# Kernel optimization log

Measured on AMD Instinct MI355X. Metric: run time of the kernel, lower is better.

## Reference

```python
import jax, jax.numpy as jnp
import numpy as np

N = 100000      # n_nodes
E = 1600000     # n_edges (avg degree 16)
F_IN = 128      # nfeat
H = 128         # nhid
C = 64          # nclass


def setup_inputs() -> dict:
    key = jax.random.key(0)
    ks = jax.random.split(key, 6)
    x = jax.random.normal(ks[0], (N, F_IN), dtype=jnp.float32)
    edge_index = jax.random.randint(ks[1], (2, E), 0, N, dtype=jnp.int32)
    # Glorot-ish init for GCNConv weights, zeros for bias (PyG default)
    W1 = jax.random.normal(ks[2], (F_IN, H), dtype=jnp.float32) * (1.0 / np.sqrt(F_IN))
    b1 = jnp.zeros((H,), dtype=jnp.float32)
    W2 = jax.random.normal(ks[3], (H, C), dtype=jnp.float32) * (1.0 / np.sqrt(H))
    b2 = jnp.zeros((C,), dtype=jnp.float32)
    return {"x": x, "edge_index": edge_index, "W1": W1, "b1": b1, "W2": W2, "b2": b2}


def _gcn_conv(x, W, b, src, dst, n):
    """PyG GCNConv: h = W^T x, out_i = sum_j norm_ij * h_j + b, with
    symmetric normalization over the self-loop-augmented graph."""
    h = x @ W                                                   # [n, out]
    deg = jax.ops.segment_sum(jnp.ones(src.shape[0], h.dtype), dst, num_segments=n)
    dinv = jnp.where(deg > 0, jax.lax.rsqrt(deg), 0.0)          # D^-1/2
    norm = dinv[src] * dinv[dst]                                # [E+n]
    msg = h[src] * norm[:, None]                                # gather + scale
    out = jax.ops.segment_sum(msg, dst, num_segments=n)         # scatter-add
    return out + b


def reference(x, edge_index, W1, b1, W2, b2):
    loop = jnp.arange(N, dtype=edge_index.dtype)
    src = jnp.concatenate([edge_index[0], loop])  # sources j (with self loops)
    dst = jnp.concatenate([edge_index[1], loop])  # targets i
    h = jax.nn.relu(_gcn_conv(x, W1, b1, src, dst, N))  # dropout = identity (eval)
    out = _gcn_conv(h, W2, b2, src, dst, N)
    return jax.nn.log_softmax(out, axis=1)
```

## Files before the change

kernel.cpp:

```cpp
#include <hip/hip_runtime.h>
#include <hip/hip_fp16.h>
#include <cstdint>
#include <cstddef>
#include <cstring>


__device__ inline unsigned pack_bf16x2(float a, float b) {
    unsigned ua = __float_as_uint(a);
    unsigned ub = __float_as_uint(b);
    ua += 0x7fffu + ((ua >> 16) & 1u);
    ub += 0x7fffu + ((ub >> 16) & 1u);
    return (ua >> 16) | (ub & 0xffff0000u);
}
__device__ inline unsigned short bf16_rne(float v) {
    unsigned u = __float_as_uint(v);
    u += 0x7fffu + ((u >> 16) & 1u);
    return (unsigned short)(u >> 16);
}
__device__ inline float bf16lo(unsigned u) { return __uint_as_float(u << 16); }
__device__ inline float bf16hi(unsigned u) { return __uint_as_float(u & 0xffff0000u); }


typedef float fv2 __attribute__((ext_vector_type(2)));

template <bool HI>
__device__ inline fv2 fp8_fv2(unsigned u) {
#if __has_builtin(__builtin_amdgcn_cvt_pk_f32_fp8)
    return __builtin_amdgcn_cvt_pk_f32_fp8((int)u, HI);
#else
    unsigned u2 = HI ? (u >> 16) : (u & 0xffffu);
    unsigned w = (u2 & 0xFFu) | ((u2 & 0xFF00u) << 8);
    unsigned hb = ((w & 0x00800080u) << 8) | ((w & 0x007f007fu) << 7);
    __half2 h2;
    memcpy(&h2, &hb, 4);
    float2 f = __half22float2(h2);
    fv2 r;
    r.x = f.x * 256.0f;
    r.y = f.y * 256.0f;
    return r;
#endif
}

__device__ inline fv2 bfpair(unsigned u) {
    union { unsigned q[2]; fv2 f; } t;
    t.q[0] = u << 16;
    t.q[1] = u & 0xffff0000u;
    return t.f;
}

__device__ inline unsigned f32_to_fp8_byte(float v) {
    unsigned short hb = __half_as_ushort(__float2half(v * 0.00390625f));
    unsigned t = hb & 0x7fffu;
    t += 0x3fu + ((t >> 7) & 1u);
    return ((hb >> 8) & 0x80u) | (t >> 7);
}

__device__ inline unsigned char f32_to_fp8_b(float v) {
#if __has_builtin(__builtin_amdgcn_cvt_pk_fp8_f32)
    return (unsigned char)(__builtin_amdgcn_cvt_pk_fp8_f32(v, v, 0, false) & 0xff);
#else
    return (unsigned char)f32_to_fp8_byte(v);
#endif
}

__device__ inline fv2 red2(fv2 v) {
    v.x += __shfl_xor(v.x, 16);
    v.y += __shfl_xor(v.y, 16);
    v.x += __shfl_xor(v.x, 32);
    v.y += __shfl_xor(v.y, 32);
    return v;
}

typedef int iv4 __attribute__((ext_vector_type(4)));

#define NPART 8
#define KB    32
#define NPP_MAX 12500


__global__ void k_zero16(int* __restrict__ p) {
    if (threadIdx.x < 16) p[threadIdx.x] = 0;
}

__global__ __launch_bounds__(256) void k_bcount(const int* __restrict__ dst,
                                                int* __restrict__ bucketCount,
                                                int E, int npp) {
    __shared__ int c8[NPART];
    if (threadIdx.x < NPART) c8[threadIdx.x] = 0;
    __syncthreads();
    int t = blockIdx.x * blockDim.x + threadIdx.x;
    int stride = gridDim.x * blockDim.x;
    int E4 = E >> 2;
    const iv4* d4 = (const iv4*)dst;
    for (int i = t; i < E4; i += stride) {
        iv4 d = d4[i];
        atomicAdd(&c8[(unsigned)d.x / (unsigned)npp], 1);
        atomicAdd(&c8[(unsigned)d.y / (unsigned)npp], 1);
        atomicAdd(&c8[(unsigned)d.z / (unsigned)npp], 1);
        atomicAdd(&c8[(unsigned)d.w / (unsigned)npp], 1);
    }
    for (int e = E4 * 4 + t; e < E; e += stride)
        atomicAdd(&c8[(unsigned)dst[e] / (unsigned)npp], 1);
    __syncthreads();
    if (threadIdx.x < NPART) atomicAdd(&bucketCount[threadIdx.x], c8[threadIdx.x]);
}

__global__ void k_bscan(const int* __restrict__ bucketCount,
                        int* __restrict__ bucketBase,
                        int* __restrict__ bucketCursor) {
    if (threadIdx.x == 0) {
        int run = 0;
        for (int p = 0; p < NPART; ++p) {
            bucketBase[p] = run;
            bucketCursor[p] = run;
            run += bucketCount[p];
        }
    }
}

__global__ __launch_bounds__(256) void k_bucket(const int* __restrict__ src,
                                                const int* __restrict__ dst,
                                                int* __restrict__ bucketCursor,
                                                int2* __restrict__ pairs,
                                                int E, int npp) {
    __shared__ int cnt8[NPART], run8[NPART], gbase8[NPART];
    int tid = threadIdx.x;
    int base_e = blockIdx.x * 4096 + tid * 16;
    int nv = min(16, E - base_e);
    if (nv < 0) nv = 0;
    int dv[16], sv[16];
    if (nv == 16) {
        for (int q = 0; q < 4; ++q) {
            iv4 d = *(const iv4*)(dst + base_e + q * 4);
            iv4 s = *(const iv4*)(src + base_e + q * 4);
            dv[q * 4 + 0] = d.x; dv[q * 4 + 1] = d.y; dv[q * 4 + 2] = d.z; dv[q * 4 + 3] = d.w;
            sv[q * 4 + 0] = s.x; sv[q * 4 + 1] = s.y; sv[q * 4 + 2] = s.z; sv[q * 4 + 3] = s.w;
        }
    } else {
        for (int k = 0; k < nv; ++k) { dv[k] = dst[base_e + k]; sv[k] = src[base_e + k]; }
    }
    if (tid < NPART) { cnt8[tid] = 0; run8[tid] = 0; }
    __syncthreads();
    for (int k = 0; k < nv; ++k)
        atomicAdd(&cnt8[(unsigned)dv[k] / (unsigned)npp], 1);
    __syncthreads();
    if (tid < NPART) gbase8[tid] = atomicAdd(&bucketCursor[tid], cnt8[tid]);
    __syncthreads();
    for (int k = 0; k < nv; ++k) {
        int p = (unsigned)dv[k] / (unsigned)npp;
        int r = atomicAdd(&run8[p], 1);
        int2 pr; pr.x = dv[k]; pr.y = sv[k];
        pairs[gbase8[p] + r] = pr;
    }
}

__global__ __launch_bounds__(256) void k_count_part(const int2* __restrict__ pairs,
                                                    const int* __restrict__ bucketBase,
                                                    const int* __restrict__ bucketCount,
                                                    int* __restrict__ cntarr, int npp) {
    __shared__ int h[NPP_MAX];
    int p = blockIdx.x & (NPART - 1);
    int b = blockIdx.x >> 3;
    int lo = p * npp;
    for (int i = threadIdx.x; i < npp; i += 256) h[i] = 0;
    __syncthreads();
    int segBase = bucketBase[p], sz = bucketCount[p];
    int chunk = (sz + KB - 1) / KB;
    int s0 = segBase + b * chunk;
    int s1 = min(segBase + sz, s0 + chunk);
    for (int i = s0 + threadIdx.x; i < s1; i += 256)
        atomicAdd(&h[pairs[i].x - lo], 1);
    __syncthreads();
    size_t out = (size_t)(p * KB + b) * npp;
    for (int i = threadIdx.x; i < npp; i += 256) cntarr[out + i] = h[i];
}

__global__ void k_indeg(const int* __restrict__ cntarr, int* __restrict__ indeg,
                        int n, int npp) {
    int d = blockIdx.x * blockDim.x + threadIdx.x;
    if (d >= n) return;
    int p = (unsigned)d / (unsigned)npp;
    int dl = d - p * npp;
    size_t base = (size_t)p * KB * npp + dl;
    int s = 0;
    for (int b = 0; b < KB; ++b) s += cntarr[base + (size_t)b * npp];
    indeg[d] = s;
}

__global__ void k_scan_local(const int* __restrict__ in, int* __restrict__ out,
                             int* __restrict__ partials, int n) {
    __shared__ int s[256];
    int t = threadIdx.x;
    int base = blockIdx.x * 1024 + t * 4;
    int v0 = (base + 0) < n ? in[base + 0] : 0;
    int v1 = (base + 1) < n ? in[base + 1] : 0;
    int v2 = (base + 2) < n ? in[base + 2] : 0;
    int v3 = (base + 3) < n ? in[base + 3] : 0;
    int sum = v0 + v1 + v2 + v3;
    s[t] = sum;
    __syncthreads();
    for (int off = 1; off < 256; off <<= 1) {
        int x = (t >= off) ? s[t - off] : 0;
        __syncthreads();
        s[t] += x;
        __syncthreads();
    }
    int excl = s[t] - sum;
    if ((base + 0) < n) out[base + 0] = excl;
    if ((base + 1) < n) out[base + 1] = excl + v0;
    if ((base + 2) < n) out[base + 2] = excl + v0 + v1;
    if ((base + 3) < n) out[base + 3] = excl + v0 + v1 + v2;
    if (t == 255) partials[blockIdx.x] = s[255];
}

__global__ void k_scan_partials(int* __restrict__ partials, int np) {
    __shared__ int s[256];
    int t = threadIdx.x;
    int v = (t < np) ? partials[t] : 0;
    s[t] = v;
    __syncthreads();
    for (int off = 1; off < 256; off <<= 1) {
        int x = (t >= off) ? s[t - off] : 0;
        __syncthreads();
        s[t] += x;
        __syncthreads();
    }
    if (t < np) partials[t] = s[t] - v;
}

__global__ void k_finalize(int* __restrict__ row_ptr, const int* __restrict__ partials,
                           const int* __restrict__ indeg, float* __restrict__ dinv,
                           int n, int E) {
    int i = blockIdx.x * blockDim.x + threadIdx.x;
    if (i < n) {
        int rp = row_ptr[i] + partials[i >> 10];
        row_ptr[i] = rp;
        dinv[i] = rsqrtf((float)indeg[i] + 1.0f);
        if (i == 0) row_ptr[n] = E;
    }
}

__global__ void k_bases(int* __restrict__ cntarr, const int* __restrict__ row_ptr,
                        int n, int npp) {
    int d = blockIdx.x * blockDim.x + threadIdx.x;
    if (d >= n) return;
    int p = (unsigned)d / (unsigned)npp;
    int dl = d - p * npp;
    size_t base = (size_t)p * KB * npp + dl;
    int run = row_ptr[d];
    for (int b = 0; b < KB; ++b) {
        size_t idx = base + (size_t)b * npp;
        int c = cntarr[idx];
        cntarr[idx] = run;
        run += c;
    }
}

__global__ __launch_bounds__(256) void k_fill2(const int2* __restrict__ pairs,
                                               const int* __restrict__ bucketBase,
                                               const int* __restrict__ bucketCount,
                                               const int* __restrict__ cntarr,
                                               int* __restrict__ col, int npp) {
    __shared__ int cur[NPP_MAX];
    int p = blockIdx.x & (NPART - 1);
    int b = blockIdx.x >> 3;
    int lo = p * npp;
    size_t slice = (size_t)(p * KB + b) * npp;
    for (int i = threadIdx.x; i < npp; i += 256) cur[i] = cntarr[slice + i];
    __syncthreads();
    int segBase = bucketBase[p], sz = bucketCount[p];
    int chunk = (sz + KB - 1) / KB;
    int s0 = segBase + b * chunk;
    int s1 = min(segBase + sz, s0 + chunk);
    for (int i = s0 + threadIdx.x; i < s1; i += 256) {
        int2 e = pairs[i];
        int pos = atomicAdd(&cur[e.x - lo], 1);
        col[pos] = e.y;
    }
}

typedef __attribute__((ext_vector_type(8))) short short8;
typedef __attribute__((ext_vector_type(4))) float f32x4;

union FragU {
    short8 s;
    uint4 u4;
    unsigned u[4];
};

template <int NOUT>
__global__ void k_packW(const float* __restrict__ W, unsigned* __restrict__ Bp) {
    const int NT = NOUT / 16;
    int nf = 4 * NT * 64;
    for (int fid = threadIdx.x; fid < nf; fid += 256) {
        int q = fid / (NT * 64);
        int rem = fid - q * NT * 64;
        int nt = rem >> 6;
        int lane = rem & 63;
        int k0 = q * 32 + (lane >> 4) * 8;
        int ncol = nt * 16 + (lane & 15);
        unsigned u[4];
        for (int h = 0; h < 4; ++h) {
            float a = W[(k0 + 2 * h) * NOUT + ncol];
            float b = W[(k0 + 2 * h + 1) * NOUT + ncol];
            u[h] = pack_bf16x2(a, b);
        }
        uint4 o = {u[0], u[1], u[2], u[3]};
        *(uint4*)(Bp + (size_t)fid * 4) = o;
    }
}

__global__ __launch_bounds__(256) void k_gemm128_mfma(const float* __restrict__ X,
                                                      const unsigned* __restrict__ Bp,
                                                      const float* __restrict__ dinv,
                                                      unsigned char* __restrict__ H8,
                                                      int n) {
    int w = threadIdx.x >> 6;
    int lane = threadIdx.x & 63;
    int quad = lane >> 4;
    int lrow = lane & 15;
    int row0 = blockIdx.x * 64 + w * 16;
    int rowA = min(row0 + lrow, n - 1);

    f32x4 acc[8];
    for (int nt = 0; nt < 8; ++nt) acc[nt] = (f32x4){0.f, 0.f, 0.f, 0.f};

    for (int q = 0; q < 4; ++q) {
        const float* xp = X + (size_t)rowA * 128 + q * 32 + quad * 8;
        float4 x0 = *(const float4*)xp;
        float4 x1 = *(const float4*)(xp + 4);
        FragU a;
        a.u[0] = pack_bf16x2(x0.x, x0.y);
        a.u[1] = pack_bf16x2(x0.z, x0.w);
        a.u[2] = pack_bf16x2(x1.x, x1.y);
        a.u[3] = pack_bf16x2(x1.z, x1.w);
        for (int nt = 0; nt < 8; ++nt) {
            FragU b;
            b.u4 = *(const uint4*)(Bp + ((size_t)(q * 8 + nt) * 64 + lane) * 4);
            acc[nt] = __builtin_amdgcn_mfma_f32_16x16x32_bf16(a.s, b.s, acc[nt], 0, 0, 0);
        }
    }

    int rbase = row0 + quad * 4;
    float dv[4];
    if (rbase + 3 < n) {
        float4 d4 = *(const float4*)(dinv + rbase);
        dv[0] = d4.x; dv[1] = d4.y; dv[2] = d4.z; dv[3] = d4.w;
    } else {
        for (int r = 0; r < 4; ++r) dv[r] = dinv[min(rbase + r, n - 1)];
    }
    for (int nt = 0; nt < 8; ++nt) {
        for (int r = 0; r < 4; ++r) {
            int row = rbase + r;
            if (row < n)
                H8[(size_t)row * 128 + nt * 16 + lrow] = f32_to_fp8_b(dv[r] * acc[nt][r]);
        }
    }
}

__global__ __launch_bounds__(256) void k_gemm64_mfma(const unsigned* __restrict__ Xb,
                                                     const unsigned* __restrict__ Bp,
                                                     const float* __restrict__ dinv,
                                                     unsigned short* __restrict__ H16,
                                                     int n) {
    int w = threadIdx.x >> 6;
    int lane = threadIdx.x & 63;
    int quad = lane >> 4;
    int lrow = lane & 15;
    int row0 = blockIdx.x * 64 + w * 16;
    int rowA = min(row0 + lrow, n - 1);

    f32x4 acc[4];
    for (int nt = 0; nt < 4; ++nt) acc[nt] = (f32x4){0.f, 0.f, 0.f, 0.f};

    for (int q = 0; q < 4; ++q) {
        FragU a;
        a.u4 = *(const uint4*)(Xb + (size_t)rowA * 64 + q * 16 + quad * 4);
        for (int nt = 0; nt < 4; ++nt) {
            FragU b;
            b.u4 = *(const uint4*)(Bp + ((size_t)(q * 4 + nt) * 64 + lane) * 4);
            acc[nt] = __builtin_amdgcn_mfma_f32_16x16x32_bf16(a.s, b.s, acc[nt], 0, 0, 0);
        }
    }

    int rbase = row0 + quad * 4;
    float dv[4];
    if (rbase + 3 < n) {
        float4 d4 = *(const float4*)(dinv + rbase);
        dv[0] = d4.x; dv[1] = d4.y; dv[2] = d4.z; dv[3] = d4.w;
    } else {
        for (int r = 0; r < 4; ++r) dv[r] = dinv[min(rbase + r, n - 1)];
    }
    for (int nt = 0; nt < 4; ++nt) {
        for (int r = 0; r < 4; ++r) {
            int row = rbase + r;
            if (row < n)
                H16[(size_t)row * 64 + nt * 16 + lrow] = bf16_rne(dv[r] * acc[nt][r]);
        }
    }
}


__global__ __launch_bounds__(256) void k_agg_relu(const unsigned* __restrict__ hs,
                                                  const float* __restrict__ dinv,
                                                  const int* __restrict__ row_ptr,
                                                  const int* __restrict__ col,
                                                  const float* __restrict__ bias,
                                                  unsigned* __restrict__ out, int n) {
    int node = blockIdx.x * 4 + (threadIdx.x >> 6);
    if (node >= n) return;
    int lane = threadIdx.x & 63;
    int q = lane >> 4;
    int l = lane & 15;
    const uint2* hrow = (const uint2*)hs;
    fv2 a0 = {0.f, 0.f}, a1 = {0.f, 0.f}, a2 = {0.f, 0.f}, a3 = {0.f, 0.f};
    if (q == 0) {
        uint2 u = hrow[(size_t)node * 16 + l];
        a0 += fp8_fv2<false>(u.x); a1 += fp8_fv2<true>(u.x);
        a2 += fp8_fv2<false>(u.y); a3 += fp8_fv2<true>(u.y);
    }
    int p0 = row_ptr[node], p1 = row_ptr[node + 1];
    for (int base = p0; base < p1; base += 64) {
        int nb = min(64, p1 - base);
        int myc = col[base + min(lane, nb - 1)];
        int k = 0;
        for (; k + 16 <= nb; k += 16) {
            int jA = __shfl(myc, k + q);
            int jB = __shfl(myc, k + 4 + q);
            int jC = __shfl(myc, k + 8 + q);
            int jD = __shfl(myc, k + 12 + q);
            uint2 uA = hrow[(size_t)jA * 16 + l];
            uint2 uB = hrow[(size_t)jB * 16 + l];
            uint2 uC = hrow[(size_t)jC * 16 + l];
            uint2 uD = hrow[(size_t)jD * 16 + l];
            a0 += fp8_fv2<false>(uA.x); a1 += fp8_fv2<true>(uA.x);
            a2 += fp8_fv2<false>(uA.y); a3 += fp8_fv2<true>(uA.y);
            a0 += fp8_fv2<false>(uB.x); a1 += fp8_fv2<true>(uB.x);
            a2 += fp8_fv2<false>(uB.y); a3 += fp8_fv2<true>(uB.y);
            a0 += fp8_fv2<false>(uC.x); a1 += fp8_fv2<true>(uC.x);
            a2 += fp8_fv2<false>(uC.y); a3 += fp8_fv2<true>(uC.y);
            a0 += fp8_fv2<false>(uD.x); a1 += fp8_fv2<true>(uD.x);
            a2 += fp8_fv2<false>(uD.y); a3 += fp8_fv2<true>(uD.y);
        }
        for (; k + 8 <= nb; k += 8) {
            int jA = __shfl(myc, k + q);
            int jB = __shfl(myc, k + 4 + q);
            uint2 uA = hrow[(size_t)jA * 16 + l];
            uint2 uB = hrow[(size_t)jB * 16 + l];
            a0 += fp8_fv2<false>(uA.x); a1 += fp8_fv2<true>(uA.x);
            a2 += fp8_fv2<false>(uA.y); a3 += fp8_fv2<true>(uA.y);
            a0 += fp8_fv2<false>(uB.x); a1 += fp8_fv2<true>(uB.x);
            a2 += fp8_fv2<false>(uB.y); a3 += fp8_fv2<true>(uB.y);
        }
        for (; k + 4 <= nb; k += 4) {
            int jA = __shfl(myc, k + q);
            uint2 uA = hrow[(size_t)jA * 16 + l];
            a0 += fp8_fv2<false>(uA.x); a1 += fp8_fv2<true>(uA.x);
            a2 += fp8_fv2<false>(uA.y); a3 += fp8_fv2<true>(uA.y);
        }
        if (k < nb) {
            int kk = k + q;
            int j = __shfl(myc, min(kk, nb - 1));
            if (kk < nb) {
                uint2 u = hrow[(size_t)j * 16 + l];
                a0 += fp8_fv2<false>(u.x); a1 += fp8_fv2<true>(u.x);
                a2 += fp8_fv2<false>(u.y); a3 += fp8_fv2<true>(u.y);
            }
        }
    }
    a0 = red2(a0); a1 = red2(a1); a2 = red2(a2); a3 = red2(a3);
    if (q == 0) {
        float di = dinv[node];
        float4 b4a = *(const float4*)(bias + 8 * l);
        float4 b4b = *(const float4*)(bias + 8 * l + 4);
        float v0 = fmaf(di, a0.x, b4a.x);
        float v1 = fmaf(di, a0.y, b4a.y);
        float v2 = fmaf(di, a1.x, b4a.z);
        float v3 = fmaf(di, a1.y, b4a.w);
        float v4 = fmaf(di, a2.x, b4b.x);
        float v5 = fmaf(di, a2.y, b4b.y);
        float v6 = fmaf(di, a3.x, b4b.z);
        float v7 = fmaf(di, a3.y, b4b.w);
        v0 = v0 > 0.f ? v0 : 0.f;
        v1 = v1 > 0.f ? v1 : 0.f;
        v2 = v2 > 0.f ? v2 : 0.f;
        v3 = v3 > 0.f ? v3 : 0.f;
        v4 = v4 > 0.f ? v4 : 0.f;
        v5 = v5 > 0.f ? v5 : 0.f;
        v6 = v6 > 0.f ? v6 : 0.f;
        v7 = v7 > 0.f ? v7 : 0.f;
        uint4 o = {pack_bf16x2(v0, v1), pack_bf16x2(v2, v3),
                   pack_bf16x2(v4, v5), pack_bf16x2(v6, v7)};
        *(uint4*)(out + (size_t)node * 64 + 4 * l) = o;
    }
}

__global__ __launch_bounds__(256) void k_agg_lsm(const unsigned* __restrict__ hs,
                                                 const float* __restrict__ dinv,
                                                 const int* __restrict__ row_ptr,
                                                 const int* __restrict__ col,
                                                 const float* __restrict__ bias,
                                                 float* __restrict__ out, int n) {
    int node = blockIdx.x * 4 + (threadIdx.x >> 6);
    if (node >= n) return;
    int lane = threadIdx.x & 63;
    int q = lane >> 4;
    int l = lane & 15;
    const uint2* hrow = (const uint2*)hs;
    fv2 aX = {0.f, 0.f}, aY = {0.f, 0.f};
    if (q == 0) {
        uint2 u = hrow[(size_t)node * 16 + l];
        aX += bfpair(u.x);
        aY += bfpair(u.y);
    }
    int p0 = row_ptr[node], p1 = row_ptr[node + 1];
    for (int base = p0; base < p1; base += 64) {
        int nb = min(64, p1 - base);
        int myc = col[base + min(lane, nb - 1)];
        int k = 0;
        for (; k + 16 <= nb; k += 16) {
            int jA = __shfl(myc, k + q);
            int jB = __shfl(myc, k + 4 + q);
            int jC = __shfl(myc, k + 8 + q);
            int jD = __shfl(myc, k + 12 + q);
            uint2 uA = hrow[(size_t)jA * 16 + l];
            uint2 uB = hrow[(size_t)jB * 16 + l];
            uint2 uC = hrow[(size_t)jC * 16 + l];
            uint2 uD = hrow[(size_t)jD * 16 + l];
            aX += bfpair(uA.x); aY += bfpair(uA.y);
            aX += bfpair(uB.x); aY += bfpair(uB.y);
            aX += bfpair(uC.x); aY += bfpair(uC.y);
            aX += bfpair(uD.x); aY += bfpair(uD.y);
        }
        for (; k + 8 <= nb; k += 8) {
            int jA = __shfl(myc, k + q);
            int jB = __shfl(myc, k + 4 + q);
            uint2 uA = hrow[(size_t)jA * 16 + l];
            uint2 uB = hrow[(size_t)jB * 16 + l];
            aX += bfpair(uA.x); aY += bfpair(uA.y);
            aX += bfpair(uB.x); aY += bfpair(uB.y);
        }
        for (; k + 4 <= nb; k += 4) {
            int jA = __shfl(myc, k + q);
            uint2 uA = hrow[(size_t)jA * 16 + l];
            aX += bfpair(uA.x); aY += bfpair(uA.y);
        }
        if (k < nb) {
            int kk = k + q;
            int j = __shfl(myc, min(kk, nb - 1));
            if (kk < nb) {
                uint2 u = hrow[(size_t)j * 16 + l];
                aX += bfpair(u.x); aY += bfpair(u.y);
            }
        }
    }
    aX = red2(aX);
    aY = red2(aY);
    float di = dinv[node];
    float4 b4 = *(const float4*)(bias + 4 * l);
    float v0 = fmaf(di, aX.x, b4.x);
    float v1 = fmaf(di, aX.y, b4.y);
    float v2 = fmaf(di, aY.x, b4.z);
    float v3 = fmaf(di, aY.y, b4.w);
    float m = fmaxf(fmaxf(v0, v1), fmaxf(v2, v3));
    for (int off = 8; off; off >>= 1) m = fmaxf(m, __shfl_xor(m, off));
    float s = __expf(v0 - m) + __expf(v1 - m) + __expf(v2 - m) + __expf(v3 - m);
    for (int off = 8; off; off >>= 1) s += __shfl_xor(s, off);
    float ls = __logf(s);
    if (q == 0) {
        float4 o = {v0 - m - ls, v1 - m - ls, v2 - m - ls, v3 - m - ls};
        *(float4*)(out + (size_t)node * 64 + 4 * l) = o;
    }
}


extern "C" void kernel_launch(void* const* d_in, const int* in_sizes, int n_in,
                              void* d_out, int out_size, void* d_ws, size_t ws_size,
                              hipStream_t stream) {
    const float* x  = (const float*)d_in[0];
    const int*   ei = (const int*)d_in[1];
    const float* W1 = (const float*)d_in[2];
    const float* b1 = (const float*)d_in[3];
    const float* W2 = (const float*)d_in[4];
    const float* b2 = (const float*)d_in[5];
    float* out = (float*)d_out;

    const int N = in_sizes[0] / 128;
    const int E = in_sizes[1] / 2;
    const int* src = ei;
    const int* dst = ei + E;
    const int npp = (N + NPART - 1) / NPART;

    char* w = (char*)d_ws;
    size_t off = 0;
    auto alloc = [&](size_t bytes) -> void* {
        void* p = w + off;
        off += (bytes + 255) & ~(size_t)255;
        return p;
    };
    int*      indeg    = (int*)alloc((size_t)N * 4);
    int*      row_ptr  = (int*)alloc((size_t)(N + 1) * 4);
    int*      colarr   = (int*)alloc((size_t)E * 4);
    int*      partials = (int*)alloc(256 * 4);
    int*      bmeta    = (int*)alloc(16 * 4);
    int*      bbase    = (int*)alloc(NPART * 4);
    float*    dinv     = (float*)alloc((size_t)N * 4);
    unsigned* h1f8     = (unsigned*)alloc((size_t)N * 32 * 4);
    unsigned* a1b      = (unsigned*)alloc((size_t)N * 64 * 4);
    unsigned* h2b      = (unsigned*)alloc((size_t)N * 32 * 4);
    unsigned* Bp1      = (unsigned*)alloc(4 * 8 * 64 * 16);
    unsigned* Bp2      = (unsigned*)alloc(4 * 4 * 64 * 16);
    int2* pairs  = (int2*)a1b;
    int*  cntarr = (int*)((char*)a1b + (size_t)E * 8);
    (void)ws_size; (void)n_in; (void)out_size;

    int* bucketCount  = bmeta;
    int* bucketCursor = bmeta + 8;
    int nscan = (N + 1023) / 1024;
    int nA3 = (E + 4095) / 4096;
    int ngemm = (N + 63) / 64;

    k_zero16<<<1, 64, 0, stream>>>(bmeta);
    k_packW<128><<<1, 256, 0, stream>>>(W1, Bp1);
    k_packW<64><<<1, 256, 0, stream>>>(W2, Bp2);
    k_bcount<<<256, 256, 0, stream>>>(dst, bucketCount, E, npp);
    k_bscan<<<1, 64, 0, stream>>>(bucketCount, bbase, bucketCursor);
    k_bucket<<<nA3, 256, 0, stream>>>(src, dst, bucketCursor, pairs, E, npp);
    k_count_part<<<NPART * KB, 256, 0, stream>>>(pairs, bbase, bucketCount, cntarr, npp);
    k_indeg<<<(N + 255) / 256, 256, 0, stream>>>(cntarr, indeg, N, npp);
    k_scan_local<<<nscan, 256, 0, stream>>>(indeg, row_ptr, partials, N);
    k_scan_partials<<<1, 256, 0, stream>>>(partials, nscan);
    k_finalize<<<(N + 255) / 256, 256, 0, stream>>>(row_ptr, partials, indeg, dinv, N, E);
    k_bases<<<(N + 255) / 256, 256, 0, stream>>>(cntarr, row_ptr, N, npp);
    k_fill2<<<NPART * KB, 256, 0, stream>>>(pairs, bbase, bucketCount, cntarr,
                                            colarr, npp);

    k_gemm128_mfma<<<ngemm, 256, 0, stream>>>(x, Bp1, dinv, (unsigned char*)h1f8, N);
    k_agg_relu<<<(N + 3) / 4, 256, 0, stream>>>(h1f8, dinv, row_ptr, colarr, b1, a1b, N);
    k_gemm64_mfma<<<ngemm, 256, 0, stream>>>(a1b, Bp2, dinv, (unsigned short*)h2b, N);
    k_agg_lsm<<<(N + 3) / 4, 256, 0, stream>>>(h2b, dinv, row_ptr, colarr, b2, out, N);
}
```

Measured before the change: 299.5 us.

## Assign one 16-lane group per node in both aggregation kernels

Both SpMM aggregation kernels now map a 16-thread group to each node instead of a full 64-lane wavefront split into four edge slices. Each group walks its own neighbor list with unrolled direct col loads, so the cross-slice shuffle reduction and the shuffled column broadcast go away and every lane writes output. Four nodes share a wavefront, which removes the idle lanes seen on low-degree nodes. The cost is divergence when nodes in one wave have unequal degrees, and less memory-level parallelism per node.

```diff
diff --git a/kernel.cpp b/kernel.cpp
--- a/kernel.cpp
+++ b/kernel.cpp
@@ -61,14 +61,6 @@
 #else
     return (unsigned char)f32_to_fp8_byte(v);
 #endif
-}
-
-__device__ inline fv2 red2(fv2 v) {
-    v.x += __shfl_xor(v.x, 16);
-    v.y += __shfl_xor(v.y, 16);
-    v.x += __shfl_xor(v.x, 32);
-    v.y += __shfl_xor(v.y, 32);
-    return v;
 }
 
 typedef int iv4 __attribute__((ext_vector_type(4)));
@@ -407,92 +399,88 @@
                                                   const int* __restrict__ col,
                                                   const float* __restrict__ bias,
                                                   unsigned* __restrict__ out, int n) {
-    int node = blockIdx.x * 4 + (threadIdx.x >> 6);
+    int node = blockIdx.x * 16 + (threadIdx.x >> 4);
     if (node >= n) return;
-    int lane = threadIdx.x & 63;
-    int q = lane >> 4;
-    int l = lane & 15;
+    int l = threadIdx.x & 15;
     const uint2* hrow = (const uint2*)hs;
     fv2 a0 = {0.f, 0.f}, a1 = {0.f, 0.f}, a2 = {0.f, 0.f}, a3 = {0.f, 0.f};
-    if (q == 0) {
+    {
         uint2 u = hrow[(size_t)node * 16 + l];
         a0 += fp8_fv2<false>(u.x); a1 += fp8_fv2<true>(u.x);
         a2 += fp8_fv2<false>(u.y); a3 += fp8_fv2<true>(u.y);
     }
-    int p0 = row_ptr[node], p1 = row_ptr[node + 1];
-    for (int base = p0; base < p1; base += 64) {
-        int nb = min(64, p1 - base);
-        int myc = col[base + min(lane, nb - 1)];
-        int k = 0;
-        for (; k + 16 <= nb; k += 16) {
-            int jA = __shfl(myc, k + q);
-            int jB = __shfl(myc, k + 4 + q);
-            int jC = __shfl(myc, k + 8 + q);
-            int jD = __shfl(myc, k + 12 + q);
-            uint2 uA = hrow[(size_t)jA * 16 + l];
-            uint2 uB = hrow[(size_t)jB * 16 + l];
-            uint2 uC = hrow[(size_t)jC * 16 + l];
-            uint2 uD = hrow[(size_t)jD * 16 + l];
-            a0 += fp8_fv2<false>(uA.x); a1 += fp8_fv2<true>(uA.x);
-            a2 += fp8_fv2<false>(uA.y); a3 += fp8_fv2<true>(uA.y);
-            a0 += fp8_fv2<false>(uB.x); a1 += fp8_fv2<true>(uB.x);
-            a2 += fp8_fv2<false>(uB.y); a3 += fp8_fv2<true>(uB.y);
-            a0 += fp8_fv2<false>(uC.x); a1 += fp8_fv2<true>(uC.x);
-            a2 += fp8_fv2<false>(uC.y); a3 += fp8_fv2<true>(uC.y);
-            a0 += fp8_fv2<false>(uD.x); a1 += fp8_fv2<true>(uD.x);
-            a2 += fp8_fv2<false>(uD.y); a3 += fp8_fv2<true>(uD.y);
-        }
-        for (; k + 8 <= nb; k += 8) {
-            int jA = __shfl(myc, k + q);
-            int jB = __shfl(myc, k + 4 + q);
-            uint2 uA = hrow[(size_t)jA * 16 + l];
-            uint2 uB = hrow[(size_t)jB * 16 + l];
-            a0 += fp8_fv2<false>(uA.x); a1 += fp8_fv2<true>(uA.x);
-            a2 += fp8_fv2<false>(uA.y); a3 += fp8_fv2<true>(uA.y);
-            a0 += fp8_fv2<false>(uB.x); a1 += fp8_fv2<true>(uB.x);
-            a2 += fp8_fv2<false>(uB.y); a3 += fp8_fv2<true>(uB.y);
-        }
-        for (; k + 4 <= nb; k += 4) {
-            int jA = __shfl(myc, k + q);
-            uint2 uA = hrow[(size_t)jA * 16 + l];
-            a0 += fp8_fv2<false>(uA.x); a1 += fp8_fv2<true>(uA.x);
-            a2 += fp8_fv2<false>(uA.y); a3 += fp8_fv2<true>(uA.y);
-        }
-        if (k < nb) {
-            int kk = k + q;
-            int j = __shfl(myc, min(kk, nb - 1));
-            if (kk < nb) {
-                uint2 u = hrow[(size_t)j * 16 + l];
-                a0 += fp8_fv2<false>(u.x); a1 += fp8_fv2<true>(u.x);
-                a2 += fp8_fv2<false>(u.y); a3 += fp8_fv2<true>(u.y);
-            }
-        }
-    }
-    a0 = red2(a0); a1 = red2(a1); a2 = red2(a2); a3 = red2(a3);
-    if (q == 0) {
-        float di = dinv[node];
-        float4 b4a = *(const float4*)(bias + 8 * l);
-        float4 b4b = *(const float4*)(bias + 8 * l + 4);
-        float v0 = fmaf(di, a0.x, b4a.x);
-        float v1 = fmaf(di, a0.y, b4a.y);
-        float v2 = fmaf(di, a1.x, b4a.z);
-        float v3 = fmaf(di, a1.y, b4a.w);
-        float v4 = fmaf(di, a2.x, b4b.x);
-        float v5 = fmaf(di, a2.y, b4b.y);
-        float v6 = fmaf(di, a3.x, b4b.z);
-        float v7 = fmaf(di, a3.y, b4b.w);
-        v0 = v0 > 0.f ? v0 : 0.f;
-        v1 = v1 > 0.f ? v1 : 0.f;
-        v2 = v2 > 0.f ? v2 : 0.f;
-        v3 = v3 > 0.f ? v3 : 0.f;
-        v4 = v4 > 0.f ? v4 : 0.f;
-        v5 = v5 > 0.f ? v5 : 0.f;
-        v6 = v6 > 0.f ? v6 : 0.f;
-        v7 = v7 > 0.f ? v7 : 0.f;
-        uint4 o = {pack_bf16x2(v0, v1), pack_bf16x2(v2, v3),
-                   pack_bf16x2(v4, v5), pack_bf16x2(v6, v7)};
-        *(uint4*)(out + (size_t)node * 64 + 4 * l) = o;
-    }
+    int k = row_ptr[node], p1 = row_ptr[node + 1];
+    for (; k + 8 <= p1; k += 8) {
+        int cA = col[k + 0], cB = col[k + 1], cC = col[k + 2], cD = col[k + 3];
+        int cE = col[k + 4], cF = col[k + 5], cG = col[k + 6], cH = col[k + 7];
+        uint2 uA = hrow[(size_t)cA * 16 + l];
+        uint2 uB = hrow[(size_t)cB * 16 + l];
+        uint2 uC = hrow[(size_t)cC * 16 + l];
+        uint2 uD = hrow[(size_t)cD * 16 + l];
+        uint2 uE = hrow[(size_t)cE * 16 + l];
+        uint2 uF = hrow[(size_t)cF * 16 + l];
+        uint2 uG = hrow[(size_t)cG * 16 + l];
+        uint2 uH = hrow[(size_t)cH * 16 + l];
+        a0 += fp8_fv2<false>(uA.x); a1 += fp8_fv2<true>(uA.x);
+        a2 += fp8_fv2<false>(uA.y); a3 += fp8_fv2<true>(uA.y);
+        a0 += fp8_fv2<false>(uB.x); a1 += fp8_fv2<true>(uB.x);
+        a2 += fp8_fv2<false>(uB.y); a3 += fp8_fv2<true>(uB.y);
+        a0 += fp8_fv2<false>(uC.x); a1 += fp8_fv2<true>(uC.x);
+        a2 += fp8_fv2<false>(uC.y); a3 += fp8_fv2<true>(uC.y);
+        a0 += fp8_fv2<false>(uD.x); a1 += fp8_fv2<true>(uD.x);
+        a2 += fp8_fv2<false>(uD.y); a3 += fp8_fv2<true>(uD.y);
+        a0 += fp8_fv2<false>(uE.x); a1 += fp8_fv2<true>(uE.x);
+        a2 += fp8_fv2<false>(uE.y); a3 += fp8_fv2<true>(uE.y);
+        a0 += fp8_fv2<false>(uF.x); a1 += fp8_fv2<true>(uF.x);
+        a2 += fp8_fv2<false>(uF.y); a3 += fp8_fv2<true>(uF.y);
+        a0 += fp8_fv2<false>(uG.x); a1 += fp8_fv2<true>(uG.x);
+        a2 += fp8_fv2<false>(uG.y); a3 += fp8_fv2<true>(uG.y);
+        a0 += fp8_fv2<false>(uH.x); a1 += fp8_fv2<true>(uH.x);
+        a2 += fp8_fv2<false>(uH.y); a3 += fp8_fv2<true>(uH.y);
+    }
+    for (; k + 4 <= p1; k += 4) {
+        int cA = col[k + 0], cB = col[k + 1], cC = col[k + 2], cD = col[k + 3];
+        uint2 uA = hrow[(size_t)cA * 16 + l];
+        uint2 uB = hrow[(size_t)cB * 16 + l];
+        uint2 uC = hrow[(size_t)cC * 16 + l];
+        uint2 uD = hrow[(size_t)cD * 16 + l];
+        a0 += fp8_fv2<false>(uA.x); a1 += fp8_fv2<true>(uA.x);
+        a2 += fp8_fv2<false>(uA.y); a3 += fp8_fv2<true>(uA.y);
+        a0 += fp8_fv2<false>(uB.x); a1 += fp8_fv2<true>(uB.x);
+        a2 += fp8_fv2<false>(uB.y); a3 += fp8_fv2<true>(uB.y);
+        a0 += fp8_fv2<false>(uC.x); a1 += fp8_fv2<true>(uC.x);
+        a2 += fp8_fv2<false>(uC.y); a3 += fp8_fv2<true>(uC.y);
+        a0 += fp8_fv2<false>(uD.x); a1 += fp8_fv2<true>(uD.x);
+        a2 += fp8_fv2<false>(uD.y); a3 += fp8_fv2<true>(uD.y);
+    }
+    for (; k < p1; ++k) {
+        int j = col[k];
+        uint2 u = hrow[(size_t)j * 16 + l];
+        a0 += fp8_fv2<false>(u.x); a1 += fp8_fv2<true>(u.x);
+        a2 += fp8_fv2<false>(u.y); a3 += fp8_fv2<true>(u.y);
+    }
+    float di = dinv[node];
+    float4 b4a = *(const float4*)(bias + 8 * l);
+    float4 b4b = *(const float4*)(bias + 8 * l + 4);
+    float v0 = fmaf(di, a0.x, b4a.x);
+    float v1 = fmaf(di, a0.y, b4a.y);
+    float v2 = fmaf(di, a1.x, b4a.z);
+    float v3 = fmaf(di, a1.y, b4a.w);
+    float v4 = fmaf(di, a2.x, b4b.x);
+    float v5 = fmaf(di, a2.y, b4b.y);
+    float v6 = fmaf(di, a3.x, b4b.z);
+    float v7 = fmaf(di, a3.y, b4b.w);
+    v0 = v0 > 0.f ? v0 : 0.f;
+    v1 = v1 > 0.f ? v1 : 0.f;
+    v2 = v2 > 0.f ? v2 : 0.f;
+    v3 = v3 > 0.f ? v3 : 0.f;
+    v4 = v4 > 0.f ? v4 : 0.f;
+    v5 = v5 > 0.f ? v5 : 0.f;
+    v6 = v6 > 0.f ? v6 : 0.f;
+    v7 = v7 > 0.f ? v7 : 0.f;
+    uint4 o = {pack_bf16x2(v0, v1), pack_bf16x2(v2, v3),
+               pack_bf16x2(v4, v5), pack_bf16x2(v6, v7)};
+    *(uint4*)(out + (size_t)node * 64 + 4 * l) = o;
 }
 
 __global__ __launch_bounds__(256) void k_agg_lsm(const unsigned* __restrict__ hs,
@@ -501,61 +489,53 @@
                                                  const int* __restrict__ col,
                                                  const float* __restrict__ bias,
                                                  float* __restrict__ out, int n) {
-    int node = blockIdx.x * 4 + (threadIdx.x >> 6);
+    int node = blockIdx.x * 16 + (threadIdx.x >> 4);
     if (node >= n) return;
-    int lane = threadIdx.x & 63;
-    int q = lane >> 4;
-    int l = lane & 15;
+    int l = threadIdx.x & 15;
     const uint2* hrow = (const uint2*)hs;
     fv2 aX = {0.f, 0.f}, aY = {0.f, 0.f};
-    if (q == 0) {
+    {
         uint2 u = hrow[(size_t)node * 16 + l];
         aX += bfpair(u.x);
         aY += bfpair(u.y);
     }
-    int p0 = row_ptr[node], p1 = row_ptr[node + 1];
-    for (int base = p0; base < p1; base += 64) {
-        int nb = min(64, p1 - base);
-        int myc = col[base + min(lane, nb - 1)];
-        int k = 0;
-        for (; k + 16 <= nb; k += 16) {
-            int jA = __shfl(myc, k + q);
-            int jB = __shfl(myc, k + 4 + q);
-            int jC = __shfl(myc, k + 8 + q);
-            int jD = __shfl(myc, k + 12 + q);
-            uint2 uA = hrow[(size_t)jA * 16 + l];
-            uint2 uB = hrow[(size_t)jB * 16 + l];
-            uint2 uC = hrow[(size_t)jC * 16 + l];
-            uint2 uD = hrow[(size_t)jD * 16 + l];
-            aX += bfpair(uA.x); aY += bfpair(uA.y);
-            aX += bfpair(uB.x); aY += bfpair(uB.y);
-            aX += bfpair(uC.x); aY += bfpair(uC.y);
-            aX += bfpair(uD.x); aY += bfpair(uD.y);
-        }
-        for (; k + 8 <= nb; k += 8) {
-            int jA = __shfl(myc, k + q);
-            int jB = __shfl(myc, k + 4 + q);
-            uint2 uA = hrow[(size_t)jA * 16 + l];
-            uint2 uB = hrow[(size_t)jB * 16 + l];
-            aX += bfpair(uA.x); aY += bfpair(uA.y);
-            aX += bfpair(uB.x); aY += bfpair(uB.y);
-        }
-        for (; k + 4 <= nb; k += 4) {
-            int jA = __shfl(myc, k + q);
-            uint2 uA = hrow[(size_t)jA * 16 + l];
-            aX += bfpair(uA.x); aY += bfpair(uA.y);
-        }
-        if (k < nb) {
-            int kk = k + q;
-            int j = __shfl(myc, min(kk, nb - 1));
-            if (kk < nb) {
-                uint2 u = hrow[(size_t)j * 16 + l];
-                aX += bfpair(u.x); aY += bfpair(u.y);
-            }
-        }
-    }
-    aX = red2(aX);
-    aY = red2(aY);
+    int k = row_ptr[node], p1 = row_ptr[node + 1];
+    for (; k + 8 <= p1; k += 8) {
+        int cA = col[k + 0], cB = col[k + 1], cC = col[k + 2], cD = col[k + 3];
+        int cE = col[k + 4], cF = col[k + 5], cG = col[k + 6], cH = col[k + 7];
+        uint2 uA = hrow[(size_t)cA * 16 + l];
+        uint2 uB = hrow[(size_t)cB * 16 + l];
+        uint2 uC = hrow[(size_t)cC * 16 + l];
+        uint2 uD = hrow[(size_t)cD * 16 + l];
+        uint2 uE = hrow[(size_t)cE * 16 + l];
+        uint2 uF = hrow[(size_t)cF * 16 + l];
+        uint2 uG = hrow[(size_t)cG * 16 + l];
+        uint2 uH = hrow[(size_t)cH * 16 + l];
+        aX += bfpair(uA.x); aY += bfpair(uA.y);
+        aX += bfpair(uB.x); aY += bfpair(uB.y);
+        aX += bfpair(uC.x); aY += bfpair(uC.y);
+        aX += bfpair(uD.x); aY += bfpair(uD.y);
+        aX += bfpair(uE.x); aY += bfpair(uE.y);
+        aX += bfpair(uF.x); aY += bfpair(uF.y);
+        aX += bfpair(uG.x); aY += bfpair(uG.y);
+        aX += bfpair(uH.x); aY += bfpair(uH.y);
+    }
+    for (; k + 4 <= p1; k += 4) {
+        int cA = col[k + 0], cB = col[k + 1], cC = col[k + 2], cD = col[k + 3];
+        uint2 uA = hrow[(size_t)cA * 16 + l];
+        uint2 uB = hrow[(size_t)cB * 16 + l];
+        uint2 uC = hrow[(size_t)cC * 16 + l];
+        uint2 uD = hrow[(size_t)cD * 16 + l];
+        aX += bfpair(uA.x); aY += bfpair(uA.y);
+        aX += bfpair(uB.x); aY += bfpair(uB.y);
+        aX += bfpair(uC.x); aY += bfpair(uC.y);
+        aX += bfpair(uD.x); aY += bfpair(uD.y);
+    }
+    for (; k < p1; ++k) {
+        int j = col[k];
+        uint2 u = hrow[(size_t)j * 16 + l];
+        aX += bfpair(u.x); aY += bfpair(u.y);
+    }
     float di = dinv[node];
     float4 b4 = *(const float4*)(bias + 4 * l);
     float v0 = fmaf(di, aX.x, b4.x);
@@ -567,10 +547,8 @@
     float s = __expf(v0 - m) + __expf(v1 - m) + __expf(v2 - m) + __expf(v3 - m);
     for (int off = 8; off; off >>= 1) s += __shfl_xor(s, off);
     float ls = __logf(s);
-    if (q == 0) {
-        float4 o = {v0 - m - ls, v1 - m - ls, v2 - m - ls, v3 - m - ls};
-        *(float4*)(out + (size_t)node * 64 + 4 * l) = o;
-    }
+    float4 o = {v0 - m - ls, v1 - m - ls, v2 - m - ls, v3 - m - ls};
+    *(float4*)(out + (size_t)node * 64 + 4 * l) = o;
 }
 
 
@@ -636,7 +614,7 @@
                                             colarr, npp);
 
     k_gemm128_mfma<<<ngemm, 256, 0, stream>>>(x, Bp1, dinv, (unsigned char*)h1f8, N);
-    k_agg_relu<<<(N + 3) / 4, 256, 0, stream>>>(h1f8, dinv, row_ptr, colarr, b1, a1b, N);
+    k_agg_relu<<<(N + 15) / 16, 256, 0, stream>>>(h1f8, dinv, row_ptr, colarr, b1, a1b, N);
     k_gemm64_mfma<<<ngemm, 256, 0, stream>>>(a1b, Bp2, dinv, (unsigned short*)h2b, N);
-    k_agg_lsm<<<(N + 3) / 4, 256, 0, stream>>>(h2b, dinv, row_ptr, colarr, b2, out, N);
-}
+    k_agg_lsm<<<(N + 15) / 16, 256, 0, stream>>>(h2b, dinv, row_ptr, colarr, b2, out, N);
+}
```

New measurement: 273.7 us. -8.6%, faster.
